# Kernel tuning notes

Measured on AMD Instinct MI355X. Metric: run time of the kernel, lower is better.

Reference implementation:

```python
import jax, jax.numpy as jnp
import numpy as np


def _bitlinear(x, W, b):
    # BitNet 1.58 absmean ternary quantization with STE.
    gamma = jnp.abs(W).mean() + 1e-8
    w_tern = jnp.clip(jnp.round(W / gamma), -1.0, 1.0)
    # STE: forward uses ternary weights, gradient flows to W.
    w_ste = w_tern + (W - jax.lax.stop_gradient(W))
    return x @ w_ste.T + b


def _gelu(x):
    return jax.nn.gelu(x, approximate=False)  # torch nn.GELU default is exact erf


def setup_inputs() -> dict:
    key = jax.random.key(0)
    ks = jax.random.split(key, 16)
    B, H = 8192, 2048
    dims = [2048, 1024, 512, 256]  # encoder: 2048->1024->512->256
    inp = {
        "z": jax.random.normal(ks[0], (B, H // 2), jnp.float32),
        "attention_out": jax.random.normal(ks[1], (B, H // 2), jnp.float32),
    }
    ki = 2
    for l in range(3):
        inp[f"We{l}"] = jax.random.normal(ks[ki], (dims[l + 1], dims[l]), jnp.float32) * 0.02
        inp[f"be{l}"] = jnp.zeros((dims[l + 1],), jnp.float32)
        ki += 1
    inp["Wb"] = jax.random.normal(ks[ki], (256, 256), jnp.float32) * 0.02
    inp["bb"] = jnp.zeros((256,), jnp.float32)
    ki += 1
    for l in range(3):  # decoder: 256->512->1024->2048
        inp[f"Wd{l}"] = jax.random.normal(ks[ki], (dims[2 - l], dims[3 - l]), jnp.float32) * 0.02
        inp[f"bd{l}"] = jnp.zeros((dims[2 - l],), jnp.float32)
        ki += 1
    return inp


def reference(z, attention_out, We0, be0, We1, be1, We2, be2, Wb, bb,
              Wd0, bd0, Wd1, bd1, Wd2, bd2):
    x = jnp.concatenate([z, attention_out], axis=-1)  # (B, 2048)
    skips = []
    for W, b in [(We0, be0), (We1, be1), (We2, be2)]:
        x = _gelu(_bitlinear(x, W, b))
        skips.append(x)
    x = _gelu(_bitlinear(x, Wb, bb))
    for i, (W, b) in enumerate([(Wd0, bd0), (Wd1, bd1), (Wd2, bd2)]):
        x = _bitlinear(x, W, b)
        skip = skips[-(i + 1)]
        if x.shape[-1] == skip.shape[-1]:  # static dim check; never true for this config
            x = x + skip
        x = _gelu(x)
    return x
```

## Files before the change

kernel.cpp:

```cpp
#include <hip/hip_runtime.h>
#include <hip/hip_bf16.h>
#include <cstdint>

typedef __attribute__((ext_vector_type(8))) __bf16 bf16x8;
typedef __attribute__((ext_vector_type(4))) float f32x4;

typedef __attribute__((address_space(1))) const void g_void;
typedef __attribute__((address_space(3))) void l_void;

__device__ __forceinline__ void gload_lds16(const void* g, void* l) {
  __builtin_amdgcn_global_load_lds((g_void*)(uintptr_t)g,
                                   (l_void*)(uint32_t)(uintptr_t)l, 16, 0, 0);
}

__device__ __forceinline__ ushort f2bf(float f) {
  union { float f; uint32_t u; } v; v.f = f;
  uint32_t r = v.u + 0x7fffu + ((v.u >> 16) & 1u);
  return (ushort)(r >> 16);
}

struct WDesc {
  const float* W[7];
  int nvec[7];
  int vcum[8];
};

__global__ void absmean_concat(WDesc wd, float* __restrict__ partials,
                               const float* __restrict__ z,
                               const float* __restrict__ att,
                               ushort* __restrict__ cat) {
  const int b = blockIdx.x;
  const int t = threadIdx.x;
  if (b < 448) {
    __shared__ float red[256];
    const int layer = b >> 6, blk = b & 63;
    const float4* W = (const float4*)wd.W[layer];
    const int nv = wd.nvec[layer];
    float s = 0.f;
    for (int i = blk * 256 + t; i < nv; i += 64 * 256) {
      float4 w = W[i];
      s += fabsf(w.x) + fabsf(w.y) + fabsf(w.z) + fabsf(w.w);
    }
    red[t] = s;
    __syncthreads();
    for (int o = 128; o > 0; o >>= 1) {
      if (t < o) red[t] += red[t + o];
      __syncthreads();
    }
    if (t == 0) partials[layer * 64 + blk] = red[0];
  } else {
    const int bc = b - 448;
    const int row = bc >> 1;
    const int h = bc & 1;
    const float* src = (h ? att : z) + (size_t)row * 1024 + t * 4;
    float4 a = *(const float4*)src;
    ushort4 o;
    o.x = f2bf(a.x); o.y = f2bf(a.y); o.z = f2bf(a.z); o.w = f2bf(a.w);
    *(ushort4*)(cat + (size_t)row * 2048 + h * 1024 + t * 4) = o;
  }
}

__global__ void quant_final(WDesc wd, const float* __restrict__ partials,
                            ushort* __restrict__ qw) {
  __shared__ float igs;
  const int t = threadIdx.x;
  const int v = blockIdx.x * 256 + t;
  const int v0 = blockIdx.x * 256;
  int layer = 0;
#pragma unroll
  for (int i = 1; i < 7; ++i) layer += (v0 >= wd.vcum[i]);
  if (t < 64) {
    float x = partials[layer * 64 + t];
    for (int o = 32; o > 0; o >>= 1) x += __shfl_down(x, o, 64);
    if (t == 0) {
      float mean = x / (float)(wd.nvec[layer] * 4);
      igs = 1.0f / (mean + 1e-8f);
    }
  }
  __syncthreads();
  if (v >= wd.vcum[7]) return;
  const float g = igs;
  const int lv = v - wd.vcum[layer];
  float4 w = ((const float4*)wd.W[layer])[lv];
  ushort4 o;
  o.x = f2bf(fmaxf(-1.f, fminf(1.f, rintf(w.x * g))));
  o.y = f2bf(fmaxf(-1.f, fminf(1.f, rintf(w.y * g))));
  o.z = f2bf(fmaxf(-1.f, fminf(1.f, rintf(w.z * g))));
  o.w = f2bf(fmaxf(-1.f, fminf(1.f, rintf(w.w * g))));
  ((ushort4*)qw)[v] = o;
}

__device__ __forceinline__ float gelu_fast(float x) {
  float x2 = x * x;
  float u = x * fmaf(x2, 0.0356774081f, 0.7978845608f);
  float e = exp2f(u * 2.8853900818f);
  float r = __builtin_amdgcn_rcpf(e + 1.0f);
  return x - x * r;
}

#define SB0() __builtin_amdgcn_sched_barrier(0)
#define BAR() __builtin_amdgcn_s_barrier()
#define VMW(NN) asm volatile("s_waitcnt vmcnt(%0)" ::"n"(NN) : "memory")

template <bool OUT_F32>
__device__ __forceinline__ void store4(void* Cv, int N, int row, int col0,
                                       const f32x4& av, const float4& bv) {
  float g0 = gelu_fast(av[0] + bv.x);
  float g1 = gelu_fast(av[1] + bv.y);
  float g2 = gelu_fast(av[2] + bv.z);
  float g3 = gelu_fast(av[3] + bv.w);
  if (OUT_F32) {
    float4 o = {g0, g1, g2, g3};
    *(float4*)&(((float*)Cv)[(size_t)row * N + col0]) = o;
  } else {
    ushort4 o;
    o.x = f2bf(g0); o.y = f2bf(g1); o.z = f2bf(g2); o.w = f2bf(g3);
    *(ushort4*)&(((ushort*)Cv)[(size_t)row * N + col0]) = o;
  }
}

template <int BN, bool OUT_F32>
__global__ __launch_bounds__(512, 2)
void gemm_pipe3(const ushort* __restrict__ A, const ushort* __restrict__ Bw,
                const float* __restrict__ bias, void* __restrict__ Cv,
                int M, int N, int K) {
  constexpr int BM = 256;
  constexpr int WN = BN / 4;
  constexpr int FM = 8;
  constexpr int FN = WN / 16;
  constexpr int HM = 4;
  constexpr int HN = 1;
  constexpr int SA = 4;
  constexpr int SB = BN / 64;
  constexpr int L = SA + SB;
  constexpr int TILE_USH = (BM + BN) * 64;

  __shared__ ushort lds[3 * TILE_USH];

  const int t = threadIdx.x;
  const int lane = t & 63, wid = t >> 6;
  const int wr = wid >> 2, wc = wid & 3;
  const int l15 = lane & 15, lhi = lane >> 4;

  const int gx = gridDim.x;
  const int nwg = gx * gridDim.y;
  int lin = blockIdx.y * gx + blockIdx.x;
  lin = (lin & 7) * (nwg >> 3) + (lin >> 3);
  const int bm0 = (lin / gx) * BM, bn0 = (lin % gx) * BN;

  const int NT = K >> 6;

  const int srow = t >> 3;
  const int scol = ((t & 7) ^ ((t >> 3) & 7)) * 8;

  auto stage = [&](int tile, int buf) {
    ushort* tb = &lds[buf * TILE_USH];
    const int kt = tile * 64;
#pragma unroll
    for (int c = 0; c < SA; ++c) {
      const int lr = c * 64 + srow;
      gload_lds16(A + (size_t)(bm0 + lr) * K + kt + scol,
                  &tb[lr * 64 + (t & 7) * 8]);
    }
#pragma unroll
    for (int c = 0; c < SB; ++c) {
      const int lr = c * 64 + srow;
      gload_lds16(Bw + (size_t)(bn0 + lr) * K + kt + scol,
                  &tb[BM * 64 + lr * 64 + (t & 7) * 8]);
    }
  };

  bf16x8 a[HM][2], b[HN][2];
  f32x4 acc[FM][FN] = {};

  auto loadA = [&](const ushort* tb, int mh) {
#pragma unroll
    for (int mi = 0; mi < HM; ++mi) {
      const int row = wr * 128 + (mh * HM + mi) * 16 + l15;
#pragma unroll
      for (int kh = 0; kh < 2; ++kh)
        a[mi][kh] =
            *(const bf16x8*)&tb[row * 64 + ((kh * 4 + lhi) ^ (l15 & 7)) * 8];
    }
  };
  auto loadB = [&](const ushort* tb, int nh) {
#pragma unroll
    for (int ni = 0; ni < HN; ++ni) {
      const int row = wc * WN + (nh * HN + ni) * 16 + l15;
#pragma unroll
      for (int kh = 0; kh < 2; ++kh)
        b[ni][kh] = *(const bf16x8*)&tb[BM * 64 + row * 64 +
                                        ((kh * 4 + lhi) ^ (l15 & 7)) * 8];
    }
  };

#define MFMA_(MH, NH)                                                        \
  {                                                                          \
    _Pragma("unroll") for (int kh = 0; kh < 2; ++kh)                         \
    _Pragma("unroll") for (int mi = 0; mi < HM; ++mi)                        \
    _Pragma("unroll") for (int ni = 0; ni < HN; ++ni)                        \
      acc[(MH) * HM + mi][(NH) * HN + ni] =                                  \
          __builtin_amdgcn_mfma_f32_16x16x32_bf16(                           \
              b[ni][kh], a[mi][kh], acc[(MH) * HM + mi][(NH) * HN + ni],     \
              0, 0, 0);                                                      \
  }

  stage(0, 0);
  stage(1, 1);
  VMW(L);
  BAR();

  int buf = 0, sbuf = 2;
  for (int tt = 0; tt < NT; ++tt) {
    const bool more = (tt + 2 < NT);
    if (more) stage(tt + 2, sbuf);
    const ushort* tb = &lds[buf * TILE_USH];
    if constexpr (FN == 2) {
      loadA(tb, 0); loadB(tb, 0);
      MFMA_(0, 0);
      loadB(tb, 1);
      MFMA_(0, 1);
      loadA(tb, 1);
      MFMA_(1, 1);
      loadB(tb, 0);
      MFMA_(1, 0);
    } else {
      loadA(tb, 0); loadB(tb, 0);
      MFMA_(0, 0);
      loadA(tb, 1);
      MFMA_(1, 0);
    }
    if (more) { VMW(L); } else { VMW(0); }
    BAR();
    buf = (buf == 2) ? 0 : buf + 1;
    sbuf = (sbuf == 2) ? 0 : sbuf + 1;
  }
#undef MFMA_

#pragma unroll
  for (int m = 0; m < FM; ++m) {
    const int row = bm0 + wr * 128 + m * 16 + l15;
#pragma unroll
    for (int n = 0; n < FN; ++n) {
      const int col0 = bn0 + wc * WN + n * 16 + lhi * 4;
      const float4 bv = *(const float4*)&bias[col0];
      store4<OUT_F32>(Cv, N, row, col0, acc[m][n], bv);
    }
  }
}

template <bool OUT_F32>
__global__ __launch_bounds__(512, 2)
void gemm_8p2(const ushort* __restrict__ A, const ushort* __restrict__ Bw,
              const float* __restrict__ bias, void* __restrict__ Cv,
              int M, int N, int K) {
  constexpr int BM = 256;
  constexpr int BN = 256;
  constexpr int TILE_USH = (BM + BN) * 64;

  __shared__ ushort lds[2 * TILE_USH];

  const int t = threadIdx.x;
  const int lane = t & 63, wid = t >> 6;
  const int wr = wid >> 2, wc = wid & 3;
  const int l15 = lane & 15, lhi = lane >> 4;

  const int gx = gridDim.x;
  const int nwg = gx * gridDim.y;
  int lin = blockIdx.y * gx + blockIdx.x;
  lin = (lin & 7) * (nwg >> 3) + (lin >> 3);
  const int bm0 = (lin / gx) * BM, bn0 = (lin % gx) * BN;

  const int NT = K >> 6;

  const int srow = t >> 3;
  const int scol = ((t & 7) ^ ((t >> 3) & 7)) * 8;

  auto stageA = [&](ushort* tb, int kt, int h) {
#pragma unroll
    for (int c = 0; c < 2; ++c) {
      const int lr = h * 128 + c * 64 + srow;
      gload_lds16(A + (size_t)(bm0 + lr) * K + kt * 64 + scol,
                  &tb[lr * 64 + (t & 7) * 8]);
    }
  };
  auto stageB = [&](ushort* tb, int kt, int h) {
#pragma unroll
    for (int c = 0; c < 2; ++c) {
      const int lr = h * 128 + c * 64 + srow;
      gload_lds16(Bw + (size_t)(bn0 + lr) * K + kt * 64 + scol,
                  &tb[BM * 64 + lr * 64 + (t & 7) * 8]);
    }
  };

  bf16x8 a[2][4][2];
  bf16x8 b[2][2][2];
  f32x4 acc[8][4] = {};

  auto loadA = [&](const ushort* tb, int mh) {
#pragma unroll
    for (int mi = 0; mi < 4; ++mi) {
      const int row = wr * 128 + mh * 64 + mi * 16 + l15;
#pragma unroll
      for (int kh = 0; kh < 2; ++kh)
        a[mh][mi][kh] =
            *(const bf16x8*)&tb[row * 64 + ((kh * 4 + lhi) ^ (l15 & 7)) * 8];
    }
  };
  auto loadB = [&](const ushort* tb, int nh) {
#pragma unroll
    for (int ni = 0; ni < 2; ++ni) {
      const int row = wc * 64 + nh * 32 + ni * 16 + l15;
#pragma unroll
      for (int kh = 0; kh < 2; ++kh)
        b[nh][ni][kh] = *(const bf16x8*)&tb[BM * 64 + row * 64 +
                                            ((kh * 4 + lhi) ^ (l15 & 7)) * 8];
    }
  };

#define MFMA_(MH, NH)                                                        \
  {                                                                          \
    __builtin_amdgcn_s_setprio(1);                                           \
    _Pragma("unroll") for (int kh = 0; kh < 2; ++kh)                         \
    _Pragma("unroll") for (int mi = 0; mi < 4; ++mi)                         \
    _Pragma("unroll") for (int ni = 0; ni < 2; ++ni)                         \
      acc[(MH) * 4 + mi][(NH) * 2 + ni] =                                    \
          __builtin_amdgcn_mfma_f32_16x16x32_bf16(                           \
              b[(NH)][ni][kh], a[(MH)][mi][kh],                              \
              acc[(MH) * 4 + mi][(NH) * 2 + ni], 0, 0, 0);                   \
    __builtin_amdgcn_s_setprio(0);                                           \
  }

  {
    ushort* b0 = &lds[0];
    ushort* b1 = &lds[TILE_USH];
    stageA(b0, 0, 0); stageA(b0, 0, 1);
    stageB(b0, 0, 0); stageB(b0, 0, 1);
    stageA(b1, 1, 0); stageA(b1, 1, 1);
    VMW(4);
    BAR();
  }

  for (int J = 0; J < NT; ++J) {
    const ushort* tb = &lds[(J & 1) * TILE_USH];
    ushort* cb = &lds[(J & 1) * TILE_USH];
    ushort* sb = &lds[((J + 1) & 1) * TILE_USH];
    const bool s1 = (J + 1) < NT;
    const bool s2 = (J + 2) < NT;

    loadA(tb, 0);
    loadB(tb, 0);
    if (s1) stageB(sb, J + 1, 0);
    MFMA_(0, 0);
    loadA(tb, 1);
    loadB(tb, 1);
    if (s1) stageB(sb, J + 1, 1);
    MFMA_(1, 1);
    SB0();
    BAR();
    if (s2) { stageA(cb, J + 2, 0); stageA(cb, J + 2, 1); }
    MFMA_(0, 1);
    MFMA_(1, 0);
    if (s2) { VMW(4); } else { VMW(0); }
    BAR();
  }
#undef MFMA_

#pragma unroll
  for (int m = 0; m < 8; ++m) {
    const int row = bm0 + wr * 128 + m * 16 + l15;
#pragma unroll
    for (int n = 0; n < 4; ++n) {
      const int col0 = bn0 + wc * 64 + n * 16 + lhi * 4;
      const float4 bv = *(const float4*)&bias[col0];
      store4<OUT_F32>(Cv, N, row, col0, acc[m][n], bv);
    }
  }
}

template <int BM, int BN, bool OUT_F32>
__global__ __launch_bounds__(256, 4)
void gemm_bt_bias_gelu(const ushort* __restrict__ A, const ushort* __restrict__ Bw,
                       const float* __restrict__ bias, void* __restrict__ Cv,
                       int M, int N, int K) {
  constexpr int WTM = BM / 32;
  constexpr int WTN = BN / 32;
  __shared__ ushort As[BM * 64];
  __shared__ ushort Bs[BN * 64];
  const int t = threadIdx.x;
  const int lane = t & 63, wid = t >> 6;
  const int wr = wid >> 1, wc = wid & 1;
  const int l15 = lane & 15, lhi = lane >> 4;

  const int gx = gridDim.x;
  const int nwg = gx * gridDim.y;
  int lin = blockIdx.y * gx + blockIdx.x;
  if ((nwg & 7) == 0) lin = (lin & 7) * (nwg >> 3) + (lin >> 3);
  const int bm0 = (lin / gx) * BM, bn0 = (lin % gx) * BN;

  const ushort* Abase = A + (size_t)bm0 * K;
  const ushort* Bbase = Bw + (size_t)bn0 * K;

  f32x4 acc[WTM][WTN] = {};

  for (int kt = 0; kt < K; kt += 64) {
#pragma unroll
    for (int i = 0; i < BM / 32; ++i) {
      int c = i * 256 + t;
      int r = c >> 3, c8 = c & 7;
      gload_lds16(Abase + (size_t)r * K + kt + c8 * 8, &As[c * 8]);
    }
#pragma unroll
    for (int i = 0; i < BN / 32; ++i) {
      int c = i * 256 + t;
      int r = c >> 3, c8 = c & 7;
      gload_lds16(Bbase + (size_t)r * K + kt + c8 * 8, &Bs[c * 8]);
    }
    asm volatile("s_waitcnt vmcnt(0)" ::: "memory");
    __syncthreads();
#pragma unroll
    for (int kk = 0; kk < 64; kk += 32) {
      bf16x8 af[WTM], bfr[WTN];
#pragma unroll
      for (int m = 0; m < WTM; ++m)
        af[m] = *(const bf16x8*)&As[(wr * (BM / 2) + m * 16 + l15) * 64 + kk + lhi * 8];
#pragma unroll
      for (int n = 0; n < WTN; ++n)
        bfr[n] = *(const bf16x8*)&Bs[(wc * (BN / 2) + n * 16 + l15) * 64 + kk + lhi * 8];
#pragma unroll
      for (int m = 0; m < WTM; ++m)
#pragma unroll
        for (int n = 0; n < WTN; ++n)
          acc[m][n] = __builtin_amdgcn_mfma_f32_16x16x32_bf16(bfr[n], af[m], acc[m][n], 0, 0, 0);
    }
    __syncthreads();
  }

#pragma unroll
  for (int m = 0; m < WTM; ++m) {
    const int row = bm0 + wr * (BM / 2) + m * 16 + l15;
#pragma unroll
    for (int n = 0; n < WTN; ++n) {
      const int col0 = bn0 + wc * (BN / 2) + n * 16 + lhi * 4;
      const float4 bv = *(const float4*)&bias[col0];
      store4<OUT_F32>(Cv, N, row, col0, acc[m][n], bv);
    }
  }
}

extern "C" void kernel_launch(void* const* d_in, const int* in_sizes, int n_in,
                              void* d_out, int out_size, void* d_ws, size_t ws_size,
                              hipStream_t stream) {
  const float* z   = (const float*)d_in[0];
  const float* att = (const float*)d_in[1];
  const float* Wptr[7] = {(const float*)d_in[2],  (const float*)d_in[4],
                          (const float*)d_in[6],  (const float*)d_in[8],
                          (const float*)d_in[10], (const float*)d_in[12],
                          (const float*)d_in[14]};
  const float* bptr[7] = {(const float*)d_in[3],  (const float*)d_in[5],
                          (const float*)d_in[7],  (const float*)d_in[9],
                          (const float*)d_in[11], (const float*)d_in[13],
                          (const float*)d_in[15]};
  const int Ns[7] = {1024, 512, 256, 256, 512, 1024, 2048};
  const int Ks[7] = {2048, 1024, 512, 256, 256, 512, 1024};
  const int M = 8192;

  char* ws = (char*)d_ws;
  ushort* bufA = (ushort*)ws;
  ushort* bufB = (ushort*)(ws + 33554432);
  ushort* qw   = (ushort*)(ws + 33554432 + 16777216);
  float* partials = (float*)(ws + 33554432 + 16777216 + 11141120);

  WDesc wd;
  int cum = 0;
  size_t qoff[7]; size_t qc = 0;
  for (int l = 0; l < 7; ++l) {
    wd.W[l] = Wptr[l];
    int nv = Ns[l] * Ks[l] / 4;
    wd.nvec[l] = nv;
    wd.vcum[l] = cum;
    cum += nv;
    qoff[l] = qc;
    qc += (size_t)Ns[l] * Ks[l];
  }
  wd.vcum[7] = cum;

  const int qblks = (cum + 255) / 256;
  absmean_concat<<<448 + 16384, 256, 0, stream>>>(wd, partials, z, att, bufA);
  quant_final<<<qblks, 256, 0, stream>>>(wd, partials, qw);

  ushort* inb = bufA; ushort* outb = bufB;
  gemm_pipe3<128, false><<<dim3(Ns[0] / 128, M / 256), dim3(512), 0, stream>>>(
      inb, qw + qoff[0], bptr[0], outb, M, Ns[0], Ks[0]);
  { ushort* tmp = inb; inb = outb; outb = tmp; }
  gemm_pipe3<64, false><<<dim3(Ns[1] / 64, M / 256), dim3(512), 0, stream>>>(
      inb, qw + qoff[1], bptr[1], outb, M, Ns[1], Ks[1]);
  { ushort* tmp = inb; inb = outb; outb = tmp; }
  gemm_bt_bias_gelu<64, 64, false><<<dim3(Ns[2] / 64, M / 64), 256, 0, stream>>>(
      inb, qw + qoff[2], bptr[2], outb, M, Ns[2], Ks[2]);
  { ushort* tmp = inb; inb = outb; outb = tmp; }
  gemm_bt_bias_gelu<64, 64, false><<<dim3(Ns[3] / 64, M / 64), 256, 0, stream>>>(
      inb, qw + qoff[3], bptr[3], outb, M, Ns[3], Ks[3]);
  { ushort* tmp = inb; inb = outb; outb = tmp; }
  gemm_pipe3<64, false><<<dim3(Ns[4] / 64, M / 256), dim3(512), 0, stream>>>(
      inb, qw + qoff[4], bptr[4], outb, M, Ns[4], Ks[4]);
  { ushort* tmp = inb; inb = outb; outb = tmp; }
  gemm_pipe3<128, false><<<dim3(Ns[5] / 128, M / 256), dim3(512), 0, stream>>>(
      inb, qw + qoff[5], bptr[5], outb, M, Ns[5], Ks[5]);
  { ushort* tmp = inb; inb = outb; outb = tmp; }
  gemm_8p2<true><<<dim3(Ns[6] / 256, M / 256), dim3(512), 0, stream>>>(
      inb, qw + qoff[6], bptr[6], d_out, M, Ns[6], Ks[6]);
}
```

Measured before the change: 176.4 us.

## Fuse 512->256 and 256->256 bitlinear layers into one kernel via LDS

Replaces the two separate GEMM launches for layers 2 and 3 with one kernel. Each block of 32 rows computes the 256-wide GELU output of layer 2, keeps it in swizzled LDS, and then multiplies it by the layer 3 weights. This removes one launch and the global round trip of the 8192x256 intermediate. In exchange, weight tiles are reloaded by all 256 blocks, there is no double buffering (it waits for vmcnt(0) every k-step), and it uses 256 threads per block with large LDS use, which may limit occupancy.

```diff
diff --git a/kernel.cpp b/kernel.cpp
--- a/kernel.cpp
+++ b/kernel.cpp
@@ -378,6 +378,93 @@
   }
 }
 
+__global__ __launch_bounds__(256, 3)
+void gemm_l2l3(const ushort* __restrict__ A, const ushort* __restrict__ W2,
+               const float* __restrict__ b2, const ushort* __restrict__ W3,
+               const float* __restrict__ b3, ushort* __restrict__ C) {
+  __shared__ ushort As[32 * 64];
+  __shared__ ushort Bs[256 * 64];
+  __shared__ ushort X[32 * 256];
+  const int t = threadIdx.x;
+  const int lane = t & 63, wid = t >> 6;
+  const int wr = wid >> 1, wc = wid & 1;
+  const int l15 = lane & 15, lhi = lane >> 4;
+  const int bm0 = blockIdx.x * 32;
+  const int arow = wr * 16 + l15;
+  const int sw = (arow & 7) << 3;
+
+  f32x4 acc[8] = {};
+
+  for (int kt = 0; kt < 512; kt += 64) {
+    {
+      int r = t >> 3, c8 = t & 7;
+      gload_lds16(A + (size_t)(bm0 + r) * 512 + kt + c8 * 8, &As[t * 8]);
+    }
+#pragma unroll
+    for (int i = 0; i < 8; ++i) {
+      int c = i * 256 + t;
+      int r = c >> 3, c8 = c & 7;
+      gload_lds16(W2 + (size_t)r * 512 + kt + c8 * 8, &Bs[c * 8]);
+    }
+    asm volatile("s_waitcnt vmcnt(0)" ::: "memory");
+    __syncthreads();
+#pragma unroll
+    for (int kk = 0; kk < 64; kk += 32) {
+      bf16x8 af = *(const bf16x8*)&As[arow * 64 + kk + lhi * 8];
+#pragma unroll
+      for (int n = 0; n < 8; ++n) {
+        bf16x8 bfr =
+            *(const bf16x8*)&Bs[(wc * 128 + n * 16 + l15) * 64 + kk + lhi * 8];
+        acc[n] = __builtin_amdgcn_mfma_f32_16x16x32_bf16(bfr, af, acc[n], 0, 0, 0);
+      }
+    }
+    __syncthreads();
+  }
+
+#pragma unroll
+  for (int n = 0; n < 8; ++n) {
+    const int col0 = wc * 128 + n * 16 + lhi * 4;
+    const float4 bv = *(const float4*)&b2[col0];
+    ushort4 o;
+    o.x = f2bf(gelu_fast(acc[n][0] + bv.x));
+    o.y = f2bf(gelu_fast(acc[n][1] + bv.y));
+    o.z = f2bf(gelu_fast(acc[n][2] + bv.z));
+    o.w = f2bf(gelu_fast(acc[n][3] + bv.w));
+    *(ushort4*)&X[arow * 256 + (col0 ^ sw)] = o;
+    acc[n][0] = 0.f; acc[n][1] = 0.f; acc[n][2] = 0.f; acc[n][3] = 0.f;
+  }
+  __syncthreads();
+
+  for (int kt = 0; kt < 256; kt += 64) {
+#pragma unroll
+    for (int i = 0; i < 8; ++i) {
+      int c = i * 256 + t;
+      int r = c >> 3, c8 = c & 7;
+      gload_lds16(W3 + (size_t)r * 256 + kt + c8 * 8, &Bs[c * 8]);
+    }
+    asm volatile("s_waitcnt vmcnt(0)" ::: "memory");
+    __syncthreads();
+#pragma unroll
+    for (int kk = 0; kk < 64; kk += 32) {
+      bf16x8 af = *(const bf16x8*)&X[arow * 256 + ((kt + kk + lhi * 8) ^ sw)];
+#pragma unroll
+      for (int n = 0; n < 8; ++n) {
+        bf16x8 bfr =
+            *(const bf16x8*)&Bs[(wc * 128 + n * 16 + l15) * 64 + kk + lhi * 8];
+        acc[n] = __builtin_amdgcn_mfma_f32_16x16x32_bf16(bfr, af, acc[n], 0, 0, 0);
+      }
+    }
+    __syncthreads();
+  }
+
+#pragma unroll
+  for (int n = 0; n < 8; ++n) {
+    const int col0 = wc * 128 + n * 16 + lhi * 4;
+    const float4 bv = *(const float4*)&b3[col0];
+    store4<false>(C, 256, bm0 + arow, col0, acc[n], bv);
+  }
+}
+
 template <int BM, int BN, bool OUT_F32>
 __global__ __launch_bounds__(256, 4)
 void gemm_bt_bias_gelu(const ushort* __restrict__ A, const ushort* __restrict__ Bw,
@@ -496,11 +583,8 @@
   gemm_pipe3<64, false><<<dim3(Ns[1] / 64, M / 256), dim3(512), 0, stream>>>(
       inb, qw + qoff[1], bptr[1], outb, M, Ns[1], Ks[1]);
   { ushort* tmp = inb; inb = outb; outb = tmp; }
-  gemm_bt_bias_gelu<64, 64, false><<<dim3(Ns[2] / 64, M / 64), 256, 0, stream>>>(
-      inb, qw + qoff[2], bptr[2], outb, M, Ns[2], Ks[2]);
-  { ushort* tmp = inb; inb = outb; outb = tmp; }
-  gemm_bt_bias_gelu<64, 64, false><<<dim3(Ns[3] / 64, M / 64), 256, 0, stream>>>(
-      inb, qw + qoff[3], bptr[3], outb, M, Ns[3], Ks[3]);
+  gemm_l2l3<<<M / 32, 256, 0, stream>>>(
+      inb, qw + qoff[2], bptr[2], qw + qoff[3], bptr[3], outb);
   { ushort* tmp = inb; inb = outb; outb = tmp; }
   gemm_pipe3<64, false><<<dim3(Ns[4] / 64, M / 256), dim3(512), 0, stream>>>(
       inb, qw + qoff[4], bptr[4], outb, M, Ns[4], Ks[4]);
```

Measured after the change: 173.9 us. No clear change (-1.4%).
